# Performance work log

Measured on AMD Instinct MI355X. Metric: run time of the kernel, lower is better.

## Reference

```python
import jax, jax.numpy as jnp
import numpy as np

N_NODES = 50000
N_EDGES = 800000
N_GRAPHS = 512
IN_DIM = 128
HIDDEN = 256
N_CLASSES = 10
MID = 12  # fixed inter-layer dim in TwoConvSAGE


def _segment_mean(x, ids, num_segments):
    s = jax.ops.segment_sum(x, ids, num_segments=num_segments)
    cnt = jax.ops.segment_sum(jnp.ones((x.shape[0],), x.dtype), ids, num_segments=num_segments)
    return jnp.where(cnt[:, None] > 0, s / jnp.maximum(cnt, 1.0)[:, None], 0.0)


def _sage_layer(h, src, dst, Wa, ba, Wb, bb):
    # copy_u + mean: mean over incoming edges of src features
    h_neigh = _segment_mean(h[src], dst, N_NODES)  # [N, d]
    h_total = jnp.concatenate([h, h_neigh], axis=1)  # [N, 2d]
    # nn.Sequential(Linear, Linear) has NO activation in between
    z = (h_total @ Wa + ba) @ Wb + bb
    return jax.nn.relu(z)  # inner F.relu; outer F.relu is idempotent


def setup_inputs() -> dict:
    key = jax.random.key(0)
    ks = jax.random.split(key, 16)
    d = {}
    d['h'] = jax.random.normal(ks[0], (N_NODES, IN_DIM), jnp.float32)
    d['src'] = jax.random.randint(ks[1], (N_EDGES,), 0, N_NODES, jnp.int32)
    d['dst'] = jax.random.randint(ks[2], (N_EDGES,), 0, N_NODES, jnp.int32)
    d['graph_id'] = jnp.sort(jax.random.randint(ks[3], (N_NODES,), 0, N_GRAPHS, jnp.int32))
    s1 = 1.0 / np.sqrt(2 * IN_DIM)
    d['W1a'] = jax.random.uniform(ks[4], (2 * IN_DIM, HIDDEN), jnp.float32, -s1, s1)
    d['b1a'] = jax.random.uniform(ks[5], (HIDDEN,), jnp.float32, -s1, s1)
    s2 = 1.0 / np.sqrt(HIDDEN)
    d['W1b'] = jax.random.uniform(ks[6], (HIDDEN, MID), jnp.float32, -s2, s2)
    d['b1b'] = jax.random.uniform(ks[7], (MID,), jnp.float32, -s2, s2)
    s3 = 1.0 / np.sqrt(2 * MID)
    d['W2a'] = jax.random.uniform(ks[8], (2 * MID, HIDDEN), jnp.float32, -s3, s3)
    d['b2a'] = jax.random.uniform(ks[9], (HIDDEN,), jnp.float32, -s3, s3)
    d['W2b'] = jax.random.uniform(ks[10], (HIDDEN, MID), jnp.float32, -s2, s2)
    d['b2b'] = jax.random.uniform(ks[11], (MID,), jnp.float32, -s2, s2)
    s4 = 1.0 / np.sqrt(MID)
    d['Wc'] = jax.random.uniform(ks[12], (MID, N_CLASSES), jnp.float32, -s4, s4)
    d['bc'] = jax.random.uniform(ks[13], (N_CLASSES,), jnp.float32, -s4, s4)
    return d


def reference(h, src, dst, graph_id, W1a, b1a, W1b, b1b, W2a, b2a, W2b, b2b, Wc, bc):
    h1 = _sage_layer(h, src, dst, W1a, b1a, W1b, b1b)   # [N, 12]
    h2 = _sage_layer(h1, src, dst, W2a, b2a, W2b, b2b)  # [N, 12]
    hg = _segment_mean(h2, graph_id, N_GRAPHS)          # [G, 12]
    return hg @ Wc + bc                                  # [G, n_classes]
```

## Files before the change

kernel.cpp:

```cpp
#include <hip/hip_runtime.h>
#include <hip/hip_bf16.h>

#define NN 50000
#define NE 800000
#define NG 512
#define NB 196
#define B1_CHUNK 2048
#define B1_BLOCKS ((NE + B1_CHUNK - 1) / B1_CHUNK)
#define CAP 5120

typedef unsigned int uint32;
typedef unsigned short ushort16;

__global__ void prep_kernel(const int* __restrict__ dst, int* __restrict__ hist_mat,
                            const float* __restrict__ W1a, const float* __restrict__ b1a,
                            const float* __restrict__ W1b, const float* __restrict__ b1b,
                            const float* __restrict__ W2a, const float* __restrict__ b2a,
                            const float* __restrict__ W2b, const float* __restrict__ b2b,
                            float* __restrict__ W1eff, float* __restrict__ b1eff,
                            float* __restrict__ W2eff, float* __restrict__ b2eff,
                            const int* __restrict__ gid, int* __restrict__ gstart) {
    int bid = blockIdx.x;
    int tid = threadIdx.x;
    if (bid < B1_BLOCKS) {
        __shared__ int hist[NB];
        for (int i = tid; i < NB; i += 256) hist[i] = 0;
        __syncthreads();
        int e0 = bid * B1_CHUNK;
        #pragma unroll
        for (int k = 0; k < 8; ++k) {
            int e = e0 + tid + k * 256;
            if (e < NE) atomicAdd(&hist[dst[e] >> 8], 1);
        }
        __syncthreads();
        int* row = hist_mat + bid * NB;
        for (int i = tid; i < NB; i += 256) row[i] = hist[i];
    } else if (bid < B1_BLOCKS + 14) {
        int t = (bid - B1_BLOCKS) * 256 + tid;
        if (t < 3072) {
            int r = t / 12, c = t % 12;
            float acc = 0.f;
            for (int k = 0; k < 256; ++k) acc += W1a[r*256 + k] * W1b[k*12 + c];
            W1eff[r*12 + c] = acc;
        } else if (t < 3084) {
            int c = t - 3072;
            float acc = b1b[c];
            for (int k = 0; k < 256; ++k) acc += b1a[k] * W1b[k*12 + c];
            b1eff[c] = acc;
        } else if (t < 3372) {
            int u = t - 3084;
            int r = u / 12, c = u % 12;
            float acc = 0.f;
            for (int k = 0; k < 256; ++k) acc += W2a[r*256 + k] * W2b[k*12 + c];
            W2eff[r*12 + c] = acc;
        } else if (t < 3384) {
            int c = t - 3372;
            float acc = b2b[c];
            for (int k = 0; k < 256; ++k) acc += b2a[k] * W2b[k*12 + c];
            b2eff[c] = acc;
        }
    } else {
        int n = (bid - B1_BLOCKS - 14) * 256 + tid;
        if (n < NN) {
            int cur = gid[n];
            int prev = (n == 0) ? -1 : gid[n - 1];
            for (int g = prev + 1; g <= cur; ++g) gstart[g] = n;
            if (n == NN - 1) {
                for (int g = cur + 1; g <= NG; ++g) gstart[g] = NN;
            }
        }
    }
}

__global__ void __launch_bounds__(768) offsp1_kernel(
    const int* __restrict__ hist_mat, int* __restrict__ off_mat, int* __restrict__ btot,
    const float* __restrict__ h, const float* __restrict__ W1eff,
    float* __restrict__ p1t, float* __restrict__ p1b) {
    __shared__ int sh[512];
    int tid = threadIdx.x;
    int b = blockIdx.x;
    int v = 0;
    if (tid < 512) {
        v = (tid < B1_BLOCKS) ? hist_mat[tid * NB + b] : 0;
        sh[tid] = v;
    }
    __syncthreads();
    for (int off = 1; off < 512; off <<= 1) {
        int t2 = (tid < 512 && tid >= off) ? sh[tid - off] : 0;
        __syncthreads();
        if (tid < 512) sh[tid] += t2;
        __syncthreads();
    }
    if (tid < B1_BLOCKS) off_mat[tid * NB + b] = sh[tid] - v;
    if (tid == B1_BLOCKS - 1) btot[b] = sh[tid];
    int n = b * 768 + tid;
    if (n >= NN) return;
    const float4* hrow = (const float4*)(h + (size_t)n * 128);
    float acc[24];
    #pragma unroll
    for (int j = 0; j < 24; ++j) acc[j] = 0.f;
    #pragma unroll 4
    for (int kq = 0; kq < 32; ++kq) {
        float4 hv = hrow[kq];
        #pragma unroll
        for (int u = 0; u < 4; ++u) {
            int k = kq * 4 + u;
            float hx = u == 0 ? hv.x : (u == 1 ? hv.y : (u == 2 ? hv.z : hv.w));
            const float4* wt = (const float4*)(W1eff + k * 12);
            const float4* wb = (const float4*)(W1eff + (128 + k) * 12);
            #pragma unroll
            for (int q = 0; q < 3; ++q) {
                float4 a = wt[q];
                float4 bq = wb[q];
                acc[q*4 + 0]      += hx * a.x;
                acc[q*4 + 1]      += hx * a.y;
                acc[q*4 + 2]      += hx * a.z;
                acc[q*4 + 3]      += hx * a.w;
                acc[12 + q*4 + 0] += hx * bq.x;
                acc[12 + q*4 + 1] += hx * bq.y;
                acc[12 + q*4 + 2] += hx * bq.z;
                acc[12 + q*4 + 3] += hx * bq.w;
            }
        }
    }
    float* pt = p1t + (size_t)n * 12;
    float* pb = p1b + (size_t)n * 12;
    #pragma unroll
    for (int c = 0; c < 12; ++c) pt[c] = acc[c];
    #pragma unroll
    for (int c = 0; c < 12; ++c) pb[c] = acc[12 + c];
}

__global__ void place_pairs_kernel(const int* __restrict__ src, const int* __restrict__ dst,
                                   const int* __restrict__ off_mat, const int* __restrict__ btot,
                                   uint32* __restrict__ pairs) {
    __shared__ int sb[256];
    __shared__ int lbase[NB];
    __shared__ int lcur[NB];
    int tid = threadIdx.x;
    int v = (tid < NB) ? btot[tid] : 0;
    sb[tid] = v;
    __syncthreads();
    for (int off = 1; off < 256; off <<= 1) {
        int t = (tid >= off) ? sb[tid - off] : 0;
        __syncthreads();
        sb[tid] += t;
        __syncthreads();
    }
    const int* orow = off_mat + blockIdx.x * NB;
    if (tid < NB) {
        lbase[tid] = (sb[tid] - v) + orow[tid];
        lcur[tid] = 0;
    }
    __syncthreads();
    int e0 = blockIdx.x * B1_CHUNK;
    #pragma unroll
    for (int k = 0; k < 8; ++k) {
        int e = e0 + tid + k * 256;
        if (e < NE) {
            int dd = dst[e];
            int ss = src[e];
            int bb = dd >> 8;
            int idx = atomicAdd(&lcur[bb], 1);
            pairs[lbase[bb] + idx] = ((uint32)ss << 8) | (uint32)(dd & 255);
        }
    }
}

__global__ void fine_gf1_kernel(const uint32* __restrict__ pairs, const int* __restrict__ btot,
                                const float* __restrict__ p1t, const float* __restrict__ p1b,
                                const float* __restrict__ b1eff, const float* __restrict__ W2eff,
                                int* __restrict__ row_start, ushort16* __restrict__ sorted_src,
                                float* __restrict__ p2t, float* __restrict__ p2b) {
    __shared__ int sb[256];
    __shared__ int cnt[256];
    __shared__ int sc[256];
    __shared__ int rs[257];
    __shared__ float hacc[256 * 13];
    __shared__ float w2[288];
    __shared__ float b1[12];
    __shared__ ushort16 ssrc[CAP];
    int tid = threadIdx.x;
    int b = blockIdx.x;
    if (tid < 256) { sb[tid] = (tid < NB) ? btot[tid] : 0; cnt[tid] = 0; }
    for (int i = tid; i < 288; i += 768) w2[i] = W2eff[i];
    if (tid >= 256 && tid < 268) b1[tid - 256] = b1eff[tid - 256];
    __syncthreads();
    for (int off = 1; off < 256; off <<= 1) {
        int t = (tid < 256 && tid >= off) ? sb[tid - off] : 0;
        __syncthreads();
        if (tid < 256) sb[tid] += t;
        __syncthreads();
    }
    int vb = btot[b];
    int R0 = sb[b] - vb, R1 = R0 + vb;
    bool use_lds = (vb <= CAP);
    for (int i = R0 + tid; i < R1; i += 768)
        atomicAdd(&cnt[(int)(pairs[i] & 255u)], 1);
    __syncthreads();
    if (tid < 256) sc[tid] = cnt[tid];
    __syncthreads();
    for (int off = 1; off < 256; off <<= 1) {
        int t = (tid < 256 && tid >= off) ? sc[tid - off] : 0;
        __syncthreads();
        if (tid < 256) sc[tid] += t;
        __syncthreads();
    }
    if (tid < 256) rs[tid] = R0 + sc[tid] - cnt[tid];
    if (tid == 255) rs[256] = R0 + sc[255];
    __syncthreads();
    if (tid < 256) cnt[tid] = 0;
    int n0 = b << 8;
    int nloc = min(256, NN - n0);
    if (tid < nloc) row_start[n0 + tid] = rs[tid];
    if (b == NB - 1 && tid == 0) row_start[NN] = R1;
    __syncthreads();
    for (int i = R0 + tid; i < R1; i += 768) {
        uint32 pr = pairs[i];
        int ln = (int)(pr & 255u);
        int ss = (int)(pr >> 8);
        int off2 = atomicAdd(&cnt[ln], 1);
        int pos = rs[ln] + off2;
        sorted_src[pos] = (ushort16)ss;
        if (use_lds) ssrc[pos - R0] = (ushort16)ss;
    }
    __syncthreads();
    {
        int li = tid / 3, q = tid - li * 3;
        int r0 = rs[li], r1 = rs[li + 1];
        float4 s = make_float4(0.f, 0.f, 0.f, 0.f);
        if (use_lds) {
            for (int i = r0 - R0; i < r1 - R0; ++i) {
                int sn = (int)ssrc[i];
                float4 v = ((const float4*)(p1b + (size_t)sn * 12))[q];
                s.x += v.x; s.y += v.y; s.z += v.z; s.w += v.w;
            }
        } else {
            for (int i = r0; i < r1; ++i) {
                int sn = (int)sorted_src[i];
                float4 v = ((const float4*)(p1b + (size_t)sn * 12))[q];
                s.x += v.x; s.y += v.y; s.z += v.z; s.w += v.w;
            }
        }
        float* hp = &hacc[li * 13 + q * 4];
        hp[0] = s.x; hp[1] = s.y; hp[2] = s.z; hp[3] = s.w;
    }
    __syncthreads();
    int n = n0 + tid;
    if (tid < 256 && n < NN) {
        int dg = rs[tid + 1] - rs[tid];
        float inv = dg > 0 ? 1.f / (float)dg : 0.f;
        const float4* ptp = (const float4*)(p1t + (size_t)n * 12);
        float4 a0 = ptp[0], a1 = ptp[1], a2 = ptp[2];
        float pt[12] = {a0.x,a0.y,a0.z,a0.w, a1.x,a1.y,a1.z,a1.w, a2.x,a2.y,a2.z,a2.w};
        float h1[12];
        #pragma unroll
        for (int j = 0; j < 12; ++j) {
            float v = pt[j] + hacc[tid * 13 + j] * inv + b1[j];
            h1[j] = v > 0.f ? v : 0.f;
        }
        float oa[12], ob[12];
        #pragma unroll
        for (int co = 0; co < 12; ++co) {
            float A = 0.f, B = 0.f;
            #pragma unroll
            for (int k = 0; k < 12; ++k) {
                A += h1[k] * w2[k*12 + co];
                B += h1[k] * w2[(12+k)*12 + co];
            }
            oa[co] = A; ob[co] = B;
        }
        float4* ot = (float4*)(p2t + (size_t)n * 12);
        float4* ou = (float4*)(p2b + (size_t)n * 12);
        ot[0] = make_float4(oa[0],oa[1],oa[2],oa[3]);
        ot[1] = make_float4(oa[4],oa[5],oa[6],oa[7]);
        ot[2] = make_float4(oa[8],oa[9],oa[10],oa[11]);
        ou[0] = make_float4(ob[0],ob[1],ob[2],ob[3]);
        ou[1] = make_float4(ob[4],ob[5],ob[6],ob[7]);
        ou[2] = make_float4(ob[8],ob[9],ob[10],ob[11]);
    }
}

__global__ void gather_fin2_kernel(const int* __restrict__ row_start,
                                   const ushort16* __restrict__ sorted_src,
                                   const float* __restrict__ p2t, const float* __restrict__ p2b,
                                   const float* __restrict__ b2eff, float* __restrict__ h2) {
    int t = blockIdx.x * blockDim.x + threadIdx.x;
    if (t >= NN * 3) return;
    int n = t / 3, q = t - n * 3;
    int r0 = row_start[n], r1 = row_start[n + 1];
    float4 s = make_float4(0.f, 0.f, 0.f, 0.f);
    if (r0 < r1) {
        int sn = (int)sorted_src[r0];
        for (int i = r0 + 1; i < r1; ++i) {
            int sn_next = (int)sorted_src[i];
            float4 v = ((const float4*)(p2b + (size_t)sn * 12))[q];
            s.x += v.x; s.y += v.y; s.z += v.z; s.w += v.w;
            sn = sn_next;
        }
        float4 v = ((const float4*)(p2b + (size_t)sn * 12))[q];
        s.x += v.x; s.y += v.y; s.z += v.z; s.w += v.w;
    }
    float inv = (r1 > r0) ? 1.f / (float)(r1 - r0) : 0.f;
    float4 pt = ((const float4*)(p2t + (size_t)n * 12))[q];
    const float* b2 = b2eff + q * 4;
    float4 o;
    o.x = pt.x + s.x * inv + b2[0]; o.x = o.x > 0.f ? o.x : 0.f;
    o.y = pt.y + s.y * inv + b2[1]; o.y = o.y > 0.f ? o.y : 0.f;
    o.z = pt.z + s.z * inv + b2[2]; o.z = o.z > 0.f ? o.z : 0.f;
    o.w = pt.w + s.w * inv + b2[3]; o.w = o.w > 0.f ? o.w : 0.f;
    ((float4*)(h2 + (size_t)n * 12))[q] = o;
}

__global__ void graph_kernel(const float* __restrict__ h2, const int* __restrict__ gstart,
                             const float* __restrict__ Wc, const float* __restrict__ bc,
                             float* __restrict__ out) {
    __shared__ float sh[252];
    __shared__ float hg[12];
    int g = blockIdx.x;
    int r0 = gstart[g], r1 = gstart[g + 1];
    int tid = threadIdx.x;
    int group = tid / 12, ch = tid - group * 12;
    if (tid < 252) {
        float s = 0.f;
        for (int n = r0 + group; n < r1; n += 21) s += h2[(size_t)n * 12 + ch];
        sh[tid] = s;
    }
    __syncthreads();
    if (tid < 12) {
        float tot = 0.f;
        #pragma unroll
        for (int k = 0; k < 21; ++k) tot += sh[k*12 + tid];
        int cntn = r1 - r0;
        hg[tid] = cntn > 0 ? tot / (float)cntn : 0.f;
    }
    __syncthreads();
    if (tid < 10) {
        float o = bc[tid];
        #pragma unroll
        for (int j = 0; j < 12; ++j) o += hg[j] * Wc[j*10 + tid];
        out[g*10 + tid] = o;
    }
}

extern "C" void kernel_launch(void* const* d_in, const int* in_sizes, int n_in,
                              void* d_out, int out_size, void* d_ws, size_t ws_size,
                              hipStream_t stream) {
    const float* h   = (const float*)d_in[0];
    const int* src   = (const int*)d_in[1];
    const int* dst   = (const int*)d_in[2];
    const int* gid   = (const int*)d_in[3];
    const float* W1a = (const float*)d_in[4];
    const float* b1a = (const float*)d_in[5];
    const float* W1b = (const float*)d_in[6];
    const float* b1b = (const float*)d_in[7];
    const float* W2a = (const float*)d_in[8];
    const float* b2a = (const float*)d_in[9];
    const float* W2b = (const float*)d_in[10];
    const float* b2b = (const float*)d_in[11];
    const float* Wc  = (const float*)d_in[12];
    const float* bc  = (const float*)d_in[13];
    float* out = (float*)d_out;

    float* ws = (float*)d_ws;
    float* W1eff = ws;
    float* b1eff = ws + 3072;
    float* W2eff = ws + 3084;
    float* b2eff = ws + 3372;
    float* p1t   = ws + 1000000;
    float* p1b   = ws + 1600000;
    float* p2t   = ws + 2200000;
    float* p2b   = ws + 2800000;
    float* h2    = ws + 3400000;
    uint32* pairs = (uint32*)(ws + 4000000);
    int*   hist_mat   = (int*)(ws + 4800000);
    int*   off_mat    = (int*)(ws + 4880000);
    ushort16* sorted_src = (ushort16*)(ws + 4960000);
    int*   row_start  = (int*)(ws + 5360000);
    int*   btot       = (int*)(ws + 5420000);
    int*   gstart     = (int*)(ws + 5424000);

    prep_kernel<<<B1_BLOCKS + 14 + 196, 256, 0, stream>>>(
        dst, hist_mat, W1a, b1a, W1b, b1b, W2a, b2a, W2b, b2b,
        W1eff, b1eff, W2eff, b2eff, gid, gstart);

    offsp1_kernel<<<NB, 768, 0, stream>>>(hist_mat, off_mat, btot, h, W1eff, p1t, p1b);

    place_pairs_kernel<<<B1_BLOCKS, 256, 0, stream>>>(src, dst, off_mat, btot, pairs);

    fine_gf1_kernel<<<NB, 768, 0, stream>>>(pairs, btot, p1t, p1b, b1eff, W2eff,
                                            row_start, sorted_src, p2t, p2b);

    gather_fin2_kernel<<<(NN * 3 + 255) / 256, 256, 0, stream>>>(row_start, sorted_src,
                                                                 p2t, p2b, b2eff, h2);

    graph_kernel<<<NG, 256, 0, stream>>>(h2, gstart, Wc, bc, out);
}
```

Baseline: 90.51 us.

## Fuse layer-2 gather with graph mean pooling via per-block segmented atomics

The layer-2 gather/finalize kernel now keeps per-node outputs in shared memory and does a segmented sum over the sorted graph ids within each block. It then atomically adds the per-graph partial sums into a zeroed accumulator, instead of writing h2 to global memory and re-reading it in a separate per-graph pooling kernel. A small output kernel applies the mean and the classifier. This removes the h2 round trip and the graph kernel's serial per-graph loops, at the cost of float atomics, which make the summation order non-deterministic, and a single serial thread per channel scanning each block's nodes.

```diff
diff --git a/kernel.cpp b/kernel.cpp
--- a/kernel.cpp
+++ b/kernel.cpp
@@ -8,6 +8,7 @@
 #define B1_CHUNK 2048
 #define B1_BLOCKS ((NE + B1_CHUNK - 1) / B1_CHUNK)
 #define CAP 5120
+#define NPB2 84
 
 typedef unsigned int uint32;
 typedef unsigned short ushort16;
@@ -19,7 +20,8 @@
                             const float* __restrict__ W2b, const float* __restrict__ b2b,
                             float* __restrict__ W1eff, float* __restrict__ b1eff,
                             float* __restrict__ W2eff, float* __restrict__ b2eff,
-                            const int* __restrict__ gid, int* __restrict__ gstart) {
+                            const int* __restrict__ gid, int* __restrict__ gstart,
+                            float* __restrict__ accg) {
     int bid = blockIdx.x;
     int tid = threadIdx.x;
     if (bid < B1_BLOCKS) {
@@ -59,7 +61,7 @@
             for (int k = 0; k < 256; ++k) acc += b2a[k] * W2b[k*12 + c];
             b2eff[c] = acc;
         }
-    } else {
+    } else if (bid < B1_BLOCKS + 14 + 196) {
         int n = (bid - B1_BLOCKS - 14) * 256 + tid;
         if (n < NN) {
             int cur = gid[n];
@@ -69,6 +71,9 @@
                 for (int g = cur + 1; g <= NG; ++g) gstart[g] = NN;
             }
         }
+    } else {
+        int t = (bid - B1_BLOCKS - 14 - 196) * 256 + tid;
+        if (t < NG * 12) accg[t] = 0.f;
     }
 }
 
@@ -281,66 +286,81 @@
     }
 }
 
-__global__ void gather_fin2_kernel(const int* __restrict__ row_start,
-                                   const ushort16* __restrict__ sorted_src,
-                                   const float* __restrict__ p2t, const float* __restrict__ p2b,
-                                   const float* __restrict__ b2eff, float* __restrict__ h2) {
+__global__ void gather_fin2_pool_kernel(const int* __restrict__ row_start,
+                                        const ushort16* __restrict__ sorted_src,
+                                        const float* __restrict__ p2t, const float* __restrict__ p2b,
+                                        const float* __restrict__ b2eff, const int* __restrict__ gid,
+                                        float* __restrict__ accg) {
+    __shared__ float poolv[NPB2 * 13];
+    __shared__ int gidl[NPB2];
+    int tid = threadIdx.x;
+    int n0 = blockIdx.x * NPB2;
+    if (tid < 252) {
+        int li = tid / 3, q = tid - li * 3;
+        int n = n0 + li;
+        if (n < NN) {
+            if (q == 0) gidl[li] = gid[n];
+            int r0 = row_start[n], r1 = row_start[n + 1];
+            float4 s = make_float4(0.f, 0.f, 0.f, 0.f);
+            if (r0 < r1) {
+                int sn = (int)sorted_src[r0];
+                for (int i = r0 + 1; i < r1; ++i) {
+                    int sn_next = (int)sorted_src[i];
+                    float4 v = ((const float4*)(p2b + (size_t)sn * 12))[q];
+                    s.x += v.x; s.y += v.y; s.z += v.z; s.w += v.w;
+                    sn = sn_next;
+                }
+                float4 v = ((const float4*)(p2b + (size_t)sn * 12))[q];
+                s.x += v.x; s.y += v.y; s.z += v.z; s.w += v.w;
+            }
+            float inv = (r1 > r0) ? 1.f / (float)(r1 - r0) : 0.f;
+            float4 pt = ((const float4*)(p2t + (size_t)n * 12))[q];
+            const float* b2 = b2eff + q * 4;
+            float* pp = &poolv[li * 13 + q * 4];
+            float o0 = pt.x + s.x * inv + b2[0];
+            float o1 = pt.y + s.y * inv + b2[1];
+            float o2 = pt.z + s.z * inv + b2[2];
+            float o3 = pt.w + s.w * inv + b2[3];
+            pp[0] = o0 > 0.f ? o0 : 0.f;
+            pp[1] = o1 > 0.f ? o1 : 0.f;
+            pp[2] = o2 > 0.f ? o2 : 0.f;
+            pp[3] = o3 > 0.f ? o3 : 0.f;
+        } else if (q == 0) {
+            gidl[li] = -1;
+        }
+    }
+    __syncthreads();
+    if (tid < 12) {
+        int ch = tid;
+        int curg = gidl[0];
+        float sum = poolv[ch];
+        for (int li = 1; li < NPB2; ++li) {
+            int g2 = gidl[li];
+            if (g2 == curg) {
+                sum += poolv[li * 13 + ch];
+            } else {
+                if (curg >= 0) atomicAdd(&accg[curg * 12 + ch], sum);
+                curg = g2;
+                if (g2 < 0) break;
+                sum = poolv[li * 13 + ch];
+            }
+        }
+        if (curg >= 0) atomicAdd(&accg[curg * 12 + ch], sum);
+    }
+}
+
+__global__ void out_kernel(const float* __restrict__ accg, const int* __restrict__ gstart,
+                           const float* __restrict__ Wc, const float* __restrict__ bc,
+                           float* __restrict__ out) {
     int t = blockIdx.x * blockDim.x + threadIdx.x;
-    if (t >= NN * 3) return;
-    int n = t / 3, q = t - n * 3;
-    int r0 = row_start[n], r1 = row_start[n + 1];
-    float4 s = make_float4(0.f, 0.f, 0.f, 0.f);
-    if (r0 < r1) {
-        int sn = (int)sorted_src[r0];
-        for (int i = r0 + 1; i < r1; ++i) {
-            int sn_next = (int)sorted_src[i];
-            float4 v = ((const float4*)(p2b + (size_t)sn * 12))[q];
-            s.x += v.x; s.y += v.y; s.z += v.z; s.w += v.w;
-            sn = sn_next;
-        }
-        float4 v = ((const float4*)(p2b + (size_t)sn * 12))[q];
-        s.x += v.x; s.y += v.y; s.z += v.z; s.w += v.w;
-    }
-    float inv = (r1 > r0) ? 1.f / (float)(r1 - r0) : 0.f;
-    float4 pt = ((const float4*)(p2t + (size_t)n * 12))[q];
-    const float* b2 = b2eff + q * 4;
-    float4 o;
-    o.x = pt.x + s.x * inv + b2[0]; o.x = o.x > 0.f ? o.x : 0.f;
-    o.y = pt.y + s.y * inv + b2[1]; o.y = o.y > 0.f ? o.y : 0.f;
-    o.z = pt.z + s.z * inv + b2[2]; o.z = o.z > 0.f ? o.z : 0.f;
-    o.w = pt.w + s.w * inv + b2[3]; o.w = o.w > 0.f ? o.w : 0.f;
-    ((float4*)(h2 + (size_t)n * 12))[q] = o;
-}
-
-__global__ void graph_kernel(const float* __restrict__ h2, const int* __restrict__ gstart,
-                             const float* __restrict__ Wc, const float* __restrict__ bc,
-                             float* __restrict__ out) {
-    __shared__ float sh[252];
-    __shared__ float hg[12];
-    int g = blockIdx.x;
-    int r0 = gstart[g], r1 = gstart[g + 1];
-    int tid = threadIdx.x;
-    int group = tid / 12, ch = tid - group * 12;
-    if (tid < 252) {
-        float s = 0.f;
-        for (int n = r0 + group; n < r1; n += 21) s += h2[(size_t)n * 12 + ch];
-        sh[tid] = s;
-    }
-    __syncthreads();
-    if (tid < 12) {
-        float tot = 0.f;
-        #pragma unroll
-        for (int k = 0; k < 21; ++k) tot += sh[k*12 + tid];
-        int cntn = r1 - r0;
-        hg[tid] = cntn > 0 ? tot / (float)cntn : 0.f;
-    }
-    __syncthreads();
-    if (tid < 10) {
-        float o = bc[tid];
-        #pragma unroll
-        for (int j = 0; j < 12; ++j) o += hg[j] * Wc[j*10 + tid];
-        out[g*10 + tid] = o;
-    }
+    if (t >= NG * 10) return;
+    int g = t / 10, cls = t - g * 10;
+    int cn = gstart[g + 1] - gstart[g];
+    float inv = cn > 0 ? 1.f / (float)cn : 0.f;
+    float o = bc[cls];
+    #pragma unroll
+    for (int j = 0; j < 12; ++j) o += accg[g*12 + j] * inv * Wc[j*10 + cls];
+    out[t] = o;
 }
 
 extern "C" void kernel_launch(void* const* d_in, const int* in_sizes, int n_in,
@@ -371,7 +391,7 @@
     float* p1b   = ws + 1600000;
     float* p2t   = ws + 2200000;
     float* p2b   = ws + 2800000;
-    float* h2    = ws + 3400000;
+    float* accg  = ws + 3400000;
     uint32* pairs = (uint32*)(ws + 4000000);
     int*   hist_mat   = (int*)(ws + 4800000);
     int*   off_mat    = (int*)(ws + 4880000);
@@ -380,9 +400,9 @@
     int*   btot       = (int*)(ws + 5420000);
     int*   gstart     = (int*)(ws + 5424000);
 
-    prep_kernel<<<B1_BLOCKS + 14 + 196, 256, 0, stream>>>(
+    prep_kernel<<<B1_BLOCKS + 14 + 196 + 24, 256, 0, stream>>>(
         dst, hist_mat, W1a, b1a, W1b, b1b, W2a, b2a, W2b, b2b,
-        W1eff, b1eff, W2eff, b2eff, gid, gstart);
+        W1eff, b1eff, W2eff, b2eff, gid, gstart, accg);
 
     offsp1_kernel<<<NB, 768, 0, stream>>>(hist_mat, off_mat, btot, h, W1eff, p1t, p1b);
 
@@ -391,8 +411,8 @@
     fine_gf1_kernel<<<NB, 768, 0, stream>>>(pairs, btot, p1t, p1b, b1eff, W2eff,
                                             row_start, sorted_src, p2t, p2b);
 
-    gather_fin2_kernel<<<(NN * 3 + 255) / 256, 256, 0, stream>>>(row_start, sorted_src,
-                                                                 p2t, p2b, b2eff, h2);
-
-    graph_kernel<<<NG, 256, 0, stream>>>(h2, gstart, Wc, bc, out);
-}
+    gather_fin2_pool_kernel<<<(NN + NPB2 - 1) / NPB2, 256, 0, stream>>>(
+        row_start, sorted_src, p2t, p2b, b2eff, gid, accg);
+
+    out_kernel<<<(NG * 10 + 255) / 256, 256, 0, stream>>>(accg, gstart, Wc, bc, out);
+}
```

Result: slower. 98.15 us (+8.4%).
